# Kernel tuning notes

Hardware: AMD Instinct MI355X
Metric: run time of the kernel (lower is better)

The kernel has to match this reference:

```python
import jax, jax.numpy as jnp
import numpy as np

N_NODES = 40000
N_EDGES = 640000
D = 128


def setup_inputs() -> dict:
    key = jax.random.key(0)
    k1, k2, k3, k4, k5 = jax.random.split(key, 5)
    x = jax.random.normal(k1, (N_NODES, D), dtype=jnp.float32)
    edge_index = jax.random.randint(k2, (2, N_EDGES), 0, N_NODES, dtype=jnp.int64)
    # torch Linear stores weight as [out, in]; xavier ~ scaled normal
    scale = (2.0 / (D + D)) ** 0.5
    W_self = jax.random.normal(k3, (D, D), dtype=jnp.float32) * scale
    W_neigh = jax.random.normal(k4, (D, D), dtype=jnp.float32) * scale
    bias = jax.random.normal(k5, (D,), dtype=jnp.float32) * 0.01
    return {"x": x, "edge_index": edge_index, "W_self": W_self,
            "W_neigh": W_neigh, "bias": bias}


def reference(x, edge_index, W_self, W_neigh, bias):
    num_nodes = x.shape[0]
    row, col = edge_index[0], edge_index[1]
    # gather source features and scatter-add into destination nodes
    agg = jax.ops.segment_sum(x[row], col, num_segments=num_nodes)  # [N, D]
    deg = jax.ops.segment_sum(jnp.ones_like(col, dtype=x.dtype), col,
                              num_segments=num_nodes)
    agg = agg / jnp.clip(deg, 1.0)[:, None]
    # h_v = lin_self(x_v) + lin_neigh(mean_u x_u) + bias  (no activation in source)
    out = x @ W_self.T + agg @ W_neigh.T + bias
    return out
```

## Files before the change

### kernel.cpp

```cpp
#include <hip/hip_runtime.h>

#define N_NODES 40000
#define N_EDGES 640000
#define D 128
#define KCAT 256
#define CAP 64
#define NXCD 8
#define PART 5000

typedef __attribute__((ext_vector_type(8))) short short8v;
typedef __attribute__((ext_vector_type(4))) float f32x4;
typedef __attribute__((ext_vector_type(2))) float f32x2;


__device__ inline unsigned short f2bf(float f) {
  union { float f; unsigned int u; } v{f};
  unsigned int r = (v.u + 0x7FFFu + ((v.u >> 16) & 1u)) >> 16;
  return (unsigned short)r;
}

__device__ inline void acc4(unsigned int v, float& a0, float& a1, float& a2,
                            float& a3) {
  f32x2 lo = __builtin_amdgcn_cvt_pk_f32_fp8(v, false);
  f32x2 hi = __builtin_amdgcn_cvt_pk_f32_fp8(v, true);
  a0 += lo.x; a1 += lo.y; a2 += hi.x; a3 += hi.y;
}

__global__ __launch_bounds__(256) void prep_kernel(
    const float* __restrict__ x, const float* __restrict__ Ws,
    const float* __restrict__ Wn, const int* __restrict__ ei,
    unsigned short* __restrict__ Wcat, unsigned int* __restrict__ x8,
    int* __restrict__ deg, unsigned short* __restrict__ slot) {
  int b = blockIdx.x;
  int t = threadIdx.x;
  int tid = b * 256 + t;
  {
    float4 v = *reinterpret_cast<const float4*>(x + (size_t)tid * 4);
    unsigned int u = __builtin_amdgcn_cvt_pk_fp8_f32(v.x, v.y, 0, false);
    u = __builtin_amdgcn_cvt_pk_fp8_f32(v.z, v.w, u, true);
    x8[tid] = u;
  }
  if (tid < 8192) {
    int j = tid >> 6;
    int kq = tid & 63;
    int k0 = kq * 4;
    float4 v = (kq < 32)
        ? *reinterpret_cast<const float4*>(Ws + j * D + k0)
        : *reinterpret_cast<const float4*>(Wn + j * D + (k0 - D));
    ushort4 h;
    h.x = f2bf(v.x); h.y = f2bf(v.y); h.z = f2bf(v.z); h.w = f2bf(v.w);
    *reinterpret_cast<ushort4*>(Wcat + j * KCAT + k0) = h;
  }
  {
    int p = b & (NXCD - 1);
    int chunk = b >> 3;
    int lo = p * PART;
    int q = chunk * 256 + t;
    int4 r = reinterpret_cast<const int4*>(ei)[q];
    int4 c = reinterpret_cast<const int4*>(ei + N_EDGES)[q];
    if ((unsigned)(c.x - lo) < PART)
      slot[(size_t)c.x * CAP + atomicAdd(&deg[c.x], 1)] = (unsigned short)r.x;
    if ((unsigned)(c.y - lo) < PART)
      slot[(size_t)c.y * CAP + atomicAdd(&deg[c.y], 1)] = (unsigned short)r.y;
    if ((unsigned)(c.z - lo) < PART)
      slot[(size_t)c.z * CAP + atomicAdd(&deg[c.z], 1)] = (unsigned short)r.z;
    if ((unsigned)(c.w - lo) < PART)
      slot[(size_t)c.w * CAP + atomicAdd(&deg[c.w], 1)] = (unsigned short)r.w;
  }
}

__global__ __launch_bounds__(256) void sage_gemm_kernel(
    const float* __restrict__ x, const unsigned int* __restrict__ x8,
    const int* __restrict__ deg, const unsigned short* __restrict__ slot,
    const unsigned short* __restrict__ Wcat, const float* __restrict__ bias,
    float* __restrict__ out) {
  __shared__ __align__(16) char Abuf[32 * 512];
  const int t = threadIdx.x;
  const int wave = t >> 6;
  const int lane = t & 63;
  const int node0 = blockIdx.x * 32;

#pragma unroll
  for (int i = 0; i < 2; ++i) {
    int q = i * 256 + t;
    int row = q >> 4;
    int s = q & 15;
    const float* xp = x + (size_t)(node0 + row) * D + s * 8;
    float4 v0 = *reinterpret_cast<const float4*>(xp);
    float4 v1 = *reinterpret_cast<const float4*>(xp + 4);
    ushort4 h0, h1;
    h0.x = f2bf(v0.x); h0.y = f2bf(v0.y); h0.z = f2bf(v0.z); h0.w = f2bf(v0.w);
    h1.x = f2bf(v1.x); h1.y = f2bf(v1.y); h1.z = f2bf(v1.z); h1.w = f2bf(v1.w);
    char* dst = Abuf + row * 512 + ((s ^ (row & 7)) << 4);
    *reinterpret_cast<ushort4*>(dst) = h0;
    *reinterpret_cast<ushort4*>(dst + 8) = h1;
  }

  {
    int hw = t >> 5;
    int l = t & 31;
#pragma unroll
    for (int pr = 0; pr < 4; ++pr) {
      int row = hw * 4 + pr;
      int node = node0 + row;
      int nd = deg[node];
      const unsigned short* sp = slot + (size_t)node * CAP;
      float a0 = 0.f, a1 = 0.f, a2 = 0.f, a3 = 0.f;
      int e = 0;
      for (; e + 8 <= nd; e += 8) {
        unsigned int v[8];
#pragma unroll
        for (int j = 0; j < 8; ++j) v[j] = x8[(size_t)sp[e + j] * 32 + l];
#pragma unroll
        for (int j = 0; j < 8; ++j) acc4(v[j], a0, a1, a2, a3);
      }
      for (; e + 4 <= nd; e += 4) {
        unsigned int v[4];
#pragma unroll
        for (int j = 0; j < 4; ++j) v[j] = x8[(size_t)sp[e + j] * 32 + l];
#pragma unroll
        for (int j = 0; j < 4; ++j) acc4(v[j], a0, a1, a2, a3);
      }
      for (; e < nd; ++e) acc4(x8[(size_t)sp[e] * 32 + l], a0, a1, a2, a3);
      float inv = 1.0f / fmaxf((float)nd, 1.0f);
      ushort4 h;
      h.x = f2bf(a0 * inv); h.y = f2bf(a1 * inv);
      h.z = f2bf(a2 * inv); h.w = f2bf(a3 * inv);
      int s = 16 + (l >> 1);
      int off = (l & 1) << 3;
      *reinterpret_cast<ushort4*>(
          Abuf + row * 512 + ((s ^ (row & 7)) << 4) + off) = h;
    }
  }
  __syncthreads();

  const int srow = lane & 15;
  const int c7 = lane & 7;
  const int sb = lane >> 4;

  f32x4 acc[2][2] = {};
#pragma unroll
  for (int ks = 0; ks < 8; ++ks) {
    short8v af[2];
#pragma unroll
    for (int mf = 0; mf < 2; ++mf) {
      int row = mf * 16 + srow;
      int sl = (ks * 4 + sb) ^ c7;
      af[mf] = *reinterpret_cast<const short8v*>(Abuf + row * 512 + (sl << 4));
    }
    short8v bf[2];
#pragma unroll
    for (int jg = 0; jg < 2; ++jg) {
      int col = wave * 32 + jg * 16 + (lane & 15);
      bf[jg] = *reinterpret_cast<const short8v*>(Wcat + (size_t)col * KCAT +
                                                 ks * 32 + sb * 8);
    }
#pragma unroll
    for (int mf = 0; mf < 2; ++mf)
#pragma unroll
      for (int jg = 0; jg < 2; ++jg)
        acc[mf][jg] = __builtin_amdgcn_mfma_f32_16x16x32_bf16(
            af[mf], bf[jg], acc[mf][jg], 0, 0, 0);
  }

#pragma unroll
  for (int jg = 0; jg < 2; ++jg) {
    int col = wave * 32 + jg * 16 + (lane & 15);
    float bv = bias[col];
#pragma unroll
    for (int mf = 0; mf < 2; ++mf) {
      int rbase = node0 + mf * 16 + (lane >> 4) * 4;
#pragma unroll
      for (int r = 0; r < 4; ++r) {
        out[(size_t)(rbase + r) * D + col] = acc[mf][jg][r] + bv;
      }
    }
  }
}

extern "C" void kernel_launch(void* const* d_in, const int* in_sizes, int n_in,
                              void* d_out, int out_size, void* d_ws, size_t ws_size,
                              hipStream_t stream) {
  const float* x    = (const float*)d_in[0];
  const int*   ei   = (const int*)d_in[1];
  const float* Ws   = (const float*)d_in[2];
  const float* Wn   = (const float*)d_in[3];
  const float* bias = (const float*)d_in[4];
  float* out = (float*)d_out;

  unsigned short* Wcat = (unsigned short*)d_ws;
  int* deg = (int*)(Wcat + 128 * KCAT);
  unsigned short* slot = (unsigned short*)(deg + N_NODES);
  unsigned int* x8 =
      (unsigned int*)(slot + (size_t)N_NODES * CAP);

  hipMemsetAsync(deg, 0, N_NODES * sizeof(int), stream);
  prep_kernel<<<5000, 256, 0, stream>>>(x, Ws, Wn, ei, Wcat, x8, deg, slot);
  sage_gemm_kernel<<<1250, 256, 0, stream>>>(x, x8, deg, slot, Wcat, bias,
                                             out);
}
```

Before: 72.23 us.

## Halve nodes per block and gather 8 bytes per lane with 16-lane groups

Each GEMM block now handles 16 nodes instead of 32, doubling the grid to 2500 blocks. In the aggregation, each node is handled by a 16-lane group reading 8 fp8 values per lane with uint2 loads, so all 16 nodes run in parallel instead of 4 sequential nodes per 32-lane group. This raises memory-level parallelism in the gather and shortens per-thread serial work. In exchange, each block reads the bf16 weight panel for half as many rows and issues half as many MFMAs per B-fragment load, so weight reuse falls.

```diff
diff --git a/kernel.cpp b/kernel.cpp
--- a/kernel.cpp
+++ b/kernel.cpp
@@ -74,17 +74,15 @@
     const int* __restrict__ deg, const unsigned short* __restrict__ slot,
     const unsigned short* __restrict__ Wcat, const float* __restrict__ bias,
     float* __restrict__ out) {
-  __shared__ __align__(16) char Abuf[32 * 512];
+  __shared__ __align__(16) char Abuf[16 * 512];
   const int t = threadIdx.x;
   const int wave = t >> 6;
   const int lane = t & 63;
-  const int node0 = blockIdx.x * 32;
+  const int node0 = blockIdx.x * 16;
 
-#pragma unroll
-  for (int i = 0; i < 2; ++i) {
-    int q = i * 256 + t;
-    int row = q >> 4;
-    int s = q & 15;
+  {
+    int row = t >> 4;
+    int s = t & 15;
     const float* xp = x + (size_t)(node0 + row) * D + s * 8;
     float4 v0 = *reinterpret_cast<const float4*>(xp);
     float4 v1 = *reinterpret_cast<const float4*>(xp + 4);
@@ -97,40 +95,48 @@
   }
 
   {
-    int hw = t >> 5;
-    int l = t & 31;
+    int g = t >> 4;
+    int l = t & 15;
+    int node = node0 + g;
+    int nd = deg[node];
+    const unsigned short* sp = slot + (size_t)node * CAP;
+    const uint2* xrow_base = reinterpret_cast<const uint2*>(x8) + l;
+    float a0 = 0.f, a1 = 0.f, a2 = 0.f, a3 = 0.f;
+    float a4 = 0.f, a5 = 0.f, a6 = 0.f, a7 = 0.f;
+    int e = 0;
+    for (; e + 8 <= nd; e += 8) {
+      uint2 v[8];
 #pragma unroll
-    for (int pr = 0; pr < 4; ++pr) {
-      int row = hw * 4 + pr;
-      int node = node0 + row;
-      int nd = deg[node];
-      const unsigned short* sp = slot + (size_t)node * CAP;
-      float a0 = 0.f, a1 = 0.f, a2 = 0.f, a3 = 0.f;
-      int e = 0;
-      for (; e + 8 <= nd; e += 8) {
-        unsigned int v[8];
+      for (int j = 0; j < 8; ++j) v[j] = xrow_base[(size_t)sp[e + j] * 16];
 #pragma unroll
-        for (int j = 0; j < 8; ++j) v[j] = x8[(size_t)sp[e + j] * 32 + l];
+      for (int j = 0; j < 8; ++j) {
+        acc4(v[j].x, a0, a1, a2, a3);
+        acc4(v[j].y, a4, a5, a6, a7);
+      }
+    }
+    for (; e + 4 <= nd; e += 4) {
+      uint2 v[4];
 #pragma unroll
-        for (int j = 0; j < 8; ++j) acc4(v[j], a0, a1, a2, a3);
+      for (int j = 0; j < 4; ++j) v[j] = xrow_base[(size_t)sp[e + j] * 16];
+#pragma unroll
+      for (int j = 0; j < 4; ++j) {
+        acc4(v[j].x, a0, a1, a2, a3);
+        acc4(v[j].y, a4, a5, a6, a7);
       }
-      for (; e + 4 <= nd; e += 4) {
-        unsigned int v[4];
-#pragma unroll
-        for (int j = 0; j < 4; ++j) v[j] = x8[(size_t)sp[e + j] * 32 + l];
-#pragma unroll
-        for (int j = 0; j < 4; ++j) acc4(v[j], a0, a1, a2, a3);
-      }
-      for (; e < nd; ++e) acc4(x8[(size_t)sp[e] * 32 + l], a0, a1, a2, a3);
-      float inv = 1.0f / fmaxf((float)nd, 1.0f);
-      ushort4 h;
-      h.x = f2bf(a0 * inv); h.y = f2bf(a1 * inv);
-      h.z = f2bf(a2 * inv); h.w = f2bf(a3 * inv);
-      int s = 16 + (l >> 1);
-      int off = (l & 1) << 3;
-      *reinterpret_cast<ushort4*>(
-          Abuf + row * 512 + ((s ^ (row & 7)) << 4) + off) = h;
     }
+    for (; e < nd; ++e) {
+      uint2 v = xrow_base[(size_t)sp[e] * 16];
+      acc4(v.x, a0, a1, a2, a3);
+      acc4(v.y, a4, a5, a6, a7);
+    }
+    float inv = 1.0f / fmaxf((float)nd, 1.0f);
+    short8v h;
+    h[0] = (short)f2bf(a0 * inv); h[1] = (short)f2bf(a1 * inv);
+    h[2] = (short)f2bf(a2 * inv); h[3] = (short)f2bf(a3 * inv);
+    h[4] = (short)f2bf(a4 * inv); h[5] = (short)f2bf(a5 * inv);
+    h[6] = (short)f2bf(a6 * inv); h[7] = (short)f2bf(a7 * inv);
+    int s = 16 + l;
+    *reinterpret_cast<short8v*>(Abuf + g * 512 + ((s ^ (g & 7)) << 4)) = h;
   }
   __syncthreads();
 
@@ -138,16 +144,12 @@
   const int c7 = lane & 7;
   const int sb = lane >> 4;
 
-  f32x4 acc[2][2] = {};
+  f32x4 acc[2] = {};
 #pragma unroll
   for (int ks = 0; ks < 8; ++ks) {
-    short8v af[2];
-#pragma unroll
-    for (int mf = 0; mf < 2; ++mf) {
-      int row = mf * 16 + srow;
-      int sl = (ks * 4 + sb) ^ c7;
-      af[mf] = *reinterpret_cast<const short8v*>(Abuf + row * 512 + (sl << 4));
-    }
+    int sl = (ks * 4 + sb) ^ c7;
+    short8v af =
+        *reinterpret_cast<const short8v*>(Abuf + srow * 512 + (sl << 4));
     short8v bf[2];
 #pragma unroll
     for (int jg = 0; jg < 2; ++jg) {
@@ -156,24 +158,19 @@
                                                  ks * 32 + sb * 8);
     }
 #pragma unroll
-    for (int mf = 0; mf < 2; ++mf)
-#pragma unroll
-      for (int jg = 0; jg < 2; ++jg)
-        acc[mf][jg] = __builtin_amdgcn_mfma_f32_16x16x32_bf16(
-            af[mf], bf[jg], acc[mf][jg], 0, 0, 0);
+    for (int jg = 0; jg < 2; ++jg)
+      acc[jg] = __builtin_amdgcn_mfma_f32_16x16x32_bf16(af, bf[jg], acc[jg],
+                                                        0, 0, 0);
   }
 
 #pragma unroll
   for (int jg = 0; jg < 2; ++jg) {
     int col = wave * 32 + jg * 16 + (lane & 15);
     float bv = bias[col];
+    int rbase = node0 + (lane >> 4) * 4;
 #pragma unroll
-    for (int mf = 0; mf < 2; ++mf) {
-      int rbase = node0 + mf * 16 + (lane >> 4) * 4;
-#pragma unroll
-      for (int r = 0; r < 4; ++r) {
-        out[(size_t)(rbase + r) * D + col] = acc[mf][jg][r] + bv;
-      }
+    for (int r = 0; r < 4; ++r) {
+      out[(size_t)(rbase + r) * D + col] = acc[jg][r] + bv;
     }
   }
 }
@@ -196,6 +193,6 @@
 
   hipMemsetAsync(deg, 0, N_NODES * sizeof(int), stream);
   prep_kernel<<<5000, 256, 0, stream>>>(x, Ws, Wn, ei, Wcat, x8, deg, slot);
-  sage_gemm_kernel<<<1250, 256, 0, stream>>>(x, x8, deg, slot, Wcat, bias,
+  sage_gemm_kernel<<<2500, 256, 0, stream>>>(x, x8, deg, slot, Wcat, bias,
                                              out);
 }
```

Result: slower. 78.07 us (+8.1%).
